# Optimization experiments

Hardware: AMD Instinct MI355X
Metric: run time of the kernel (lower is better)

The kernel has to match this reference:

```python
import jax, jax.numpy as jnp
import numpy as np

N, M, D, E = 16384, 8192, 8, 2_000_000
DELTA = 1.0   # init arg delta
P = 1.0       # init arg p (forced to 1 in __init__)
EPS = 1e-6


def setup_inputs() -> dict:
    key = jax.random.key(0)
    ks = jax.random.split(key, 7)
    return {
        "gamma_rows": jax.random.normal(ks[0], (N,), dtype=jnp.float32),
        "gamma_cols": jax.random.normal(ks[1], (M,), dtype=jnp.float32),
        "latent_z": jax.random.uniform(ks[2], (N, D), dtype=jnp.float32),
        "latent_w": jax.random.uniform(ks[3], (M, D), dtype=jnp.float32),
        "weights": jax.random.uniform(ks[4], (E,), dtype=jnp.float32),
        "rows_idx": jax.random.randint(ks[5], (E,), 0, N, dtype=jnp.int32),
        "col_idx": jax.random.randint(ks[6], (E,), 0, M, dtype=jnp.int32),
    }


def reference(gamma_rows, gamma_cols, latent_z, latent_w, weights, rows_idx, col_idx):
    # Simplex projections (Softmax over latent dim)
    z = jax.nn.softmax(latent_z, axis=1)   # [N, D]
    w = jax.nn.softmax(latent_w, axis=1)   # [M, D]

    # torch.cdist(z, w, p=2): full N x M euclidean distance matrix
    sq = (jnp.sum(z * z, axis=1)[:, None]
          + jnp.sum(w * w, axis=1)[None, :]
          - 2.0 * (z @ w.T))                       # [N, M]
    dist = jnp.sqrt(jnp.maximum(sq, 0.0))          # [N, M]
    dist_matrix = -DELTA * (dist + EPS)            # [N, M]

    # z_pdist1 = exp(gamma_rows) @ exp(dist_matrix) @ exp(gamma_cols)
    z_pdist1 = jnp.einsum("i,ij,j->", jnp.exp(gamma_rows),
                          jnp.exp(dist_matrix), jnp.exp(gamma_cols))

    # Edge (link) term: per-edge euclidean distance between gathered embeddings
    delta_latent = jnp.sqrt(jnp.sum((z[rows_idx] - w[col_idx]) ** 2, axis=-1))  # [E]
    z_pdist2 = jnp.sum(weights * (gamma_rows[rows_idx] + gamma_cols[col_idx]
                                  - (DELTA * delta_latent) ** P))

    return -z_pdist2 + z_pdist1
```

## Files before the change

kernel.cpp:

```cpp
#include <hip/hip_runtime.h>
#include <math.h>

#define N_ROWS 16384
#define M_COLS 8192
#define TPB 256
#define IT 4
#define JT 128
#define NJ (M_COLS / JT)
#define NIB (N_ROWS / (TPB * IT))
#define PAIR_BLOCKS (NIB * NJ)
#define EDGE_BLOCKS 1024
#define FUSED_BLOCKS (PAIR_BLOCKS + EDGE_BLOCKS)

typedef float v2f __attribute__((ext_vector_type(2)));

#define LOG2E 1.4426950408889634f
#define C2 2.0813689810056077f

__global__ __launch_bounds__(TPB) void rownorm_kernel(
    const float* __restrict__ lz, const float* __restrict__ gr,
    const float* __restrict__ lw, const float* __restrict__ gc,
    float* __restrict__ z, float* __restrict__ zz, float* __restrict__ eg,
    float* __restrict__ w, float* __restrict__ ww, float* __restrict__ ec)
{
    int gi = blockIdx.x * TPB + threadIdx.x;
    const float *src, *g;
    float *dv, *dq, *de;
    int i;
    if (gi < N_ROWS) { src = lz; g = gr; dv = z; dq = zz; de = eg; i = gi; }
    else             { src = lw; g = gc; dv = w; dq = ww; de = ec; i = gi - N_ROWS; }

    const float4* sp = (const float4*)(src + (size_t)i * 8);
    float4 a = sp[0], b = sp[1];
    float v[8] = {a.x, a.y, a.z, a.w, b.x, b.y, b.z, b.w};
    float m = v[0];
    #pragma unroll
    for (int d = 1; d < 8; d++) m = fmaxf(m, v[d]);
    float s = 0.f;
    #pragma unroll
    for (int d = 0; d < 8; d++) { v[d] = __expf(v[d] - m); s += v[d]; }
    float inv = 1.f / s;
    float sq = 0.f;
    #pragma unroll
    for (int d = 0; d < 8; d++) { v[d] *= inv; sq = fmaf(v[d], v[d], sq); }
    float4 o0 = {v[0], v[1], v[2], v[3]};
    float4 o1 = {v[4], v[5], v[6], v[7]};
    float4* dp = (float4*)(dv + (size_t)i * 8);
    dp[0] = o0; dp[1] = o1;
    dq[i] = C2 * sq;
    de[i] = __expf(g[i]);
}

__global__ __launch_bounds__(TPB) void fused_kernel(
    const float* __restrict__ z, const float* __restrict__ zz,
    const float* __restrict__ eg,
    const float* __restrict__ w, const float* __restrict__ ww,
    const float* __restrict__ ec,
    const float* __restrict__ gr, const float* __restrict__ gc,
    const float* __restrict__ wt,
    const int* __restrict__ ridx, const int* __restrict__ cidx, int E,
    double* __restrict__ pair_part, double* __restrict__ edge_part)
{
    __shared__ float  sw[JT * 8];
    __shared__ float  swq[JT];
    __shared__ float  sec[JT];
    __shared__ double sred[TPB];

    const int t   = threadIdx.x;
    const int rid = blockIdx.x >> 1;

    if ((blockIdx.x & 1) == 0) {
        const int ib = rid / NJ;
        const int jb = rid - ib * NJ;
        const int j0 = jb * JT;

        ((float4*)sw)[t] = ((const float4*)(w + (size_t)j0 * 8))[t];
        if (t < JT) { swq[t] = ww[j0 + t]; sec[t] = ec[j0 + t]; }

        v2f  zi[IT][4];
        float zzi[IT], acc[IT];
        const int ibase = ib * (TPB * IT);
        #pragma unroll
        for (int k = 0; k < IT; k++) {
            int i = ibase + k * TPB + t;
            const float4* zp = (const float4*)(z + (size_t)i * 8);
            float4 a = zp[0], b = zp[1];
            zi[k][0] = (v2f){-2.f * C2 * a.x, -2.f * C2 * a.y};
            zi[k][1] = (v2f){-2.f * C2 * a.z, -2.f * C2 * a.w};
            zi[k][2] = (v2f){-2.f * C2 * b.x, -2.f * C2 * b.y};
            zi[k][3] = (v2f){-2.f * C2 * b.z, -2.f * C2 * b.w};
            zzi[k] = zz[i];
            acc[k] = 0.f;
        }
        __syncthreads();

        for (int j = 0; j < JT; j++) {
            float4 wa = ((const float4*)sw)[j * 2];
            float4 wb = ((const float4*)sw)[j * 2 + 1];
            v2f w01 = {wa.x, wa.y}, w23 = {wa.z, wa.w};
            v2f w45 = {wb.x, wb.y}, w67 = {wb.z, wb.w};
            float wq = swq[j];
            float e  = sec[j];
            #pragma unroll
            for (int k = 0; k < IT; k++) {
                v2f p = {zzi[k], wq};
                p = __builtin_elementwise_fma(zi[k][0], w01, p);
                p = __builtin_elementwise_fma(zi[k][1], w23, p);
                p = __builtin_elementwise_fma(zi[k][2], w45, p);
                p = __builtin_elementwise_fma(zi[k][3], w67, p);
                float sq = fmaxf(p.x + p.y, 0.f);
                float d, pr;
                asm("v_sqrt_f32 %0, %1" : "=v"(d) : "v"(sq));
                asm("v_exp_f32 %0, -%1" : "=v"(pr) : "v"(d));
                acc[k] = fmaf(e, pr, acc[k]);
            }
        }

        double tp = 0.0;
        #pragma unroll
        for (int k = 0; k < IT; k++) {
            int i = ibase + k * TPB + t;
            tp += (double)eg[i] * (double)acc[k];
        }

        sred[t] = tp;
        __syncthreads();
        for (int s = TPB / 2; s > 0; s >>= 1) {
            if (t < s) sred[t] += sred[t + s];
            __syncthreads();
        }
        if (t == 0) pair_part[rid] = sred[0];
    } else {
        int tid = rid * TPB + t;
        const int stride = EDGE_BLOCKS * TPB;
        double local = 0.0;
        #pragma unroll 2
        for (int e = tid; e < E; e += stride) {
            int r = ridx[e], c = cidx[e];
            const float4* zp = (const float4*)(z + (size_t)r * 8);
            const float4* wp = (const float4*)(w + (size_t)c * 8);
            float4 za = zp[0], zb = zp[1], wa = wp[0], wb = wp[1];
            float d0 = za.x - wa.x, d1 = za.y - wa.y, d2 = za.z - wa.z, d3 = za.w - wa.w;
            float d4 = zb.x - wb.x, d5 = zb.y - wb.y, d6 = zb.z - wb.z, d7 = zb.w - wb.w;
            float s = d0 * d0;
            s = fmaf(d1, d1, s); s = fmaf(d2, d2, s); s = fmaf(d3, d3, s);
            s = fmaf(d4, d4, s); s = fmaf(d5, d5, s); s = fmaf(d6, d6, s);
            s = fmaf(d7, d7, s);
            float dist;
            asm("v_sqrt_f32 %0, %1" : "=v"(dist) : "v"(s));
            local += (double)(wt[e] * (gr[r] + gc[c] - dist));
        }
        sred[t] = local;
        __syncthreads();
        for (int s2 = TPB / 2; s2 > 0; s2 >>= 1) {
            if (t < s2) sred[t] += sred[t + s2];
            __syncthreads();
        }
        if (t == 0) edge_part[rid] = sred[0];
    }
}

__global__ __launch_bounds__(TPB) void final_kernel(
    const double* __restrict__ pp, int np,
    const double* __restrict__ ep, int ne,
    float* __restrict__ out)
{
    __shared__ double sred[TPB];
    const int t = threadIdx.x;
    double s1 = 0.0, s2 = 0.0;
    for (int i = t; i < np; i += TPB) s1 += pp[i];
    for (int i = t; i < ne; i += TPB) s2 += ep[i];
    sred[t] = s1;
    __syncthreads();
    for (int s = TPB / 2; s > 0; s >>= 1) {
        if (t < s) sred[t] += sred[t + s];
        __syncthreads();
    }
    double pair_sum = sred[0];
    __syncthreads();
    sred[t] = s2;
    __syncthreads();
    for (int s = TPB / 2; s > 0; s >>= 1) {
        if (t < s) sred[t] += sred[t + s];
        __syncthreads();
    }
    if (t == 0) {
        double edge_sum = sred[0];
        double cf = exp(-1.0e-6);
        out[0] = (float)(cf * pair_sum - edge_sum);
    }
}

extern "C" void kernel_launch(void* const* d_in, const int* in_sizes, int n_in,
                              void* d_out, int out_size, void* d_ws, size_t ws_size,
                              hipStream_t stream)
{
    const float* gamma_rows = (const float*)d_in[0];
    const float* gamma_cols = (const float*)d_in[1];
    const float* latent_z   = (const float*)d_in[2];
    const float* latent_w   = (const float*)d_in[3];
    const float* weights    = (const float*)d_in[4];
    const int*   rows_idx   = (const int*)d_in[5];
    const int*   col_idx    = (const int*)d_in[6];
    float* out = (float*)d_out;
    const int E = in_sizes[4];

    char* base = (char*)d_ws;
    size_t off = 0;
    float* z  = (float*)(base + off); off += (size_t)N_ROWS * 8 * 4;
    float* zz = (float*)(base + off); off += (size_t)N_ROWS * 4;
    float* eg = (float*)(base + off); off += (size_t)N_ROWS * 4;
    float* w  = (float*)(base + off); off += (size_t)M_COLS * 8 * 4;
    float* ww = (float*)(base + off); off += (size_t)M_COLS * 4;
    float* ec = (float*)(base + off); off += (size_t)M_COLS * 4;
    double* pair_part = (double*)(base + off); off += (size_t)PAIR_BLOCKS * 8;
    double* edge_part = (double*)(base + off); off += (size_t)EDGE_BLOCKS * 8;
    (void)ws_size;

    rownorm_kernel<<<(N_ROWS + M_COLS) / TPB, TPB, 0, stream>>>(
        latent_z, gamma_rows, latent_w, gamma_cols, z, zz, eg, w, ww, ec);
    fused_kernel<<<FUSED_BLOCKS, TPB, 0, stream>>>(
        z, zz, eg, w, ww, ec, gamma_rows, gamma_cols,
        weights, rows_idx, col_idx, E, pair_part, edge_part);
    final_kernel<<<1, TPB, 0, stream>>>(pair_part, PAIR_BLOCKS,
                                        edge_part, EDGE_BLOCKS, out);
}
```

Measured before the change: 173.4 us.

## Gather half-precision embeddings for edges, unroll edge loop, prefetch pair LDS reads

The row-normalisation kernel now also writes FP16 copies of the softmaxed embeddings. The edge path gathers those, with four edges per thread through vector loads of the index, weight and gamma values, so each random gather fetches half the bytes and more loads are in flight at once. Blocks are now interleaved one pair block to two edge blocks, and edge blocks double to 2048 so a single pass covers all edges. The pair loop prefetches the next column's shared-memory values and splits the FMA chain to shorten the dependency. The cost is FP16 rounding error in per-edge distances, and the single-pass edge path assumes E fits the grid and is a multiple of four.

Result: no change. 173.6 us (+0.1%).

```diff
diff --git a/kernel.cpp b/kernel.cpp
--- a/kernel.cpp
+++ b/kernel.cpp
@@ -9,26 +9,30 @@
 #define NJ (M_COLS / JT)
 #define NIB (N_ROWS / (TPB * IT))
 #define PAIR_BLOCKS (NIB * NJ)
-#define EDGE_BLOCKS 1024
-#define FUSED_BLOCKS (PAIR_BLOCKS + EDGE_BLOCKS)
+#define EDGE_BLOCKS 2048
+#define EU 4
+#define GRID_BLOCKS (PAIR_BLOCKS + EDGE_BLOCKS)
 
 typedef float v2f __attribute__((ext_vector_type(2)));
-
-#define LOG2E 1.4426950408889634f
+typedef _Float16 h8 __attribute__((ext_vector_type(8)));
+
 #define C2 2.0813689810056077f
 
 __global__ __launch_bounds__(TPB) void rownorm_kernel(
     const float* __restrict__ lz, const float* __restrict__ gr,
     const float* __restrict__ lw, const float* __restrict__ gc,
     float* __restrict__ z, float* __restrict__ zz, float* __restrict__ eg,
-    float* __restrict__ w, float* __restrict__ ww, float* __restrict__ ec)
+    _Float16* __restrict__ zh,
+    float* __restrict__ w, float* __restrict__ ww, float* __restrict__ ec,
+    _Float16* __restrict__ wh)
 {
     int gi = blockIdx.x * TPB + threadIdx.x;
     const float *src, *g;
     float *dv, *dq, *de;
+    _Float16* dh;
     int i;
-    if (gi < N_ROWS) { src = lz; g = gr; dv = z; dq = zz; de = eg; i = gi; }
-    else             { src = lw; g = gc; dv = w; dq = ww; de = ec; i = gi - N_ROWS; }
+    if (gi < N_ROWS) { src = lz; g = gr; dv = z; dq = zz; de = eg; dh = zh; i = gi; }
+    else             { src = lw; g = gc; dv = w; dq = ww; de = ec; dh = wh; i = gi - N_ROWS; }
 
     const float4* sp = (const float4*)(src + (size_t)i * 8);
     float4 a = sp[0], b = sp[1];
@@ -41,12 +45,18 @@
     for (int d = 0; d < 8; d++) { v[d] = __expf(v[d] - m); s += v[d]; }
     float inv = 1.f / s;
     float sq = 0.f;
+    h8 hv;
     #pragma unroll
-    for (int d = 0; d < 8; d++) { v[d] *= inv; sq = fmaf(v[d], v[d], sq); }
+    for (int d = 0; d < 8; d++) {
+        v[d] *= inv;
+        sq = fmaf(v[d], v[d], sq);
+        hv[d] = (_Float16)v[d];
+    }
     float4 o0 = {v[0], v[1], v[2], v[3]};
     float4 o1 = {v[4], v[5], v[6], v[7]};
     float4* dp = (float4*)(dv + (size_t)i * 8);
     dp[0] = o0; dp[1] = o1;
+    *(h8*)(dh + (size_t)i * 8) = hv;
     dq[i] = C2 * sq;
     de[i] = __expf(g[i]);
 }
@@ -56,6 +66,7 @@
     const float* __restrict__ eg,
     const float* __restrict__ w, const float* __restrict__ ww,
     const float* __restrict__ ec,
+    const _Float16* __restrict__ zh, const _Float16* __restrict__ wh,
     const float* __restrict__ gr, const float* __restrict__ gc,
     const float* __restrict__ wt,
     const int* __restrict__ ridx, const int* __restrict__ cidx, int E,
@@ -66,10 +77,13 @@
     __shared__ float  sec[JT];
     __shared__ double sred[TPB];
 
-    const int t   = threadIdx.x;
-    const int rid = blockIdx.x >> 1;
-
-    if ((blockIdx.x & 1) == 0) {
+    const int t     = threadIdx.x;
+    const int bid   = blockIdx.x;
+    const int third = bid / 3;
+    const int rem   = bid - third * 3;
+
+    if (rem == 0) {
+        const int rid = third;
         const int ib = rid / NJ;
         const int jb = rid - ib * NJ;
         const int j0 = jb * JT;
@@ -94,26 +108,31 @@
         }
         __syncthreads();
 
+        const float4* s4 = (const float4*)sw;
+        float4 wa = s4[0], wb = s4[1];
+        float wq = swq[0], e = sec[0];
         for (int j = 0; j < JT; j++) {
-            float4 wa = ((const float4*)sw)[j * 2];
-            float4 wb = ((const float4*)sw)[j * 2 + 1];
+            const int jn = (j + 1) & (JT - 1);
+            float4 wan = s4[jn * 2], wbn = s4[jn * 2 + 1];
+            float wqn = swq[jn], en = sec[jn];
+
             v2f w01 = {wa.x, wa.y}, w23 = {wa.z, wa.w};
             v2f w45 = {wb.x, wb.y}, w67 = {wb.z, wb.w};
-            float wq = swq[j];
-            float e  = sec[j];
             #pragma unroll
             for (int k = 0; k < IT; k++) {
                 v2f p = {zzi[k], wq};
                 p = __builtin_elementwise_fma(zi[k][0], w01, p);
                 p = __builtin_elementwise_fma(zi[k][1], w23, p);
-                p = __builtin_elementwise_fma(zi[k][2], w45, p);
-                p = __builtin_elementwise_fma(zi[k][3], w67, p);
+                v2f q = zi[k][2] * w45;
+                q = __builtin_elementwise_fma(zi[k][3], w67, q);
+                p += q;
                 float sq = fmaxf(p.x + p.y, 0.f);
                 float d, pr;
                 asm("v_sqrt_f32 %0, %1" : "=v"(d) : "v"(sq));
                 asm("v_exp_f32 %0, -%1" : "=v"(pr) : "v"(d));
                 acc[k] = fmaf(e, pr, acc[k]);
             }
+            wa = wan; wb = wbn; wq = wqn; e = en;
         }
 
         double tp = 0.0;
@@ -131,24 +150,39 @@
         }
         if (t == 0) pair_part[rid] = sred[0];
     } else {
-        int tid = rid * TPB + t;
-        const int stride = EDGE_BLOCKS * TPB;
+        const int erank = 2 * third + (rem - 1);
+        const int tid = erank * TPB + t;
+        const int e0 = tid * EU;
         double local = 0.0;
-        #pragma unroll 2
-        for (int e = tid; e < E; e += stride) {
-            int r = ridx[e], c = cidx[e];
-            const float4* zp = (const float4*)(z + (size_t)r * 8);
-            const float4* wp = (const float4*)(w + (size_t)c * 8);
-            float4 za = zp[0], zb = zp[1], wa = wp[0], wb = wp[1];
-            float d0 = za.x - wa.x, d1 = za.y - wa.y, d2 = za.z - wa.z, d3 = za.w - wa.w;
-            float d4 = zb.x - wb.x, d5 = zb.y - wb.y, d6 = zb.z - wb.z, d7 = zb.w - wb.w;
-            float s = d0 * d0;
-            s = fmaf(d1, d1, s); s = fmaf(d2, d2, s); s = fmaf(d3, d3, s);
-            s = fmaf(d4, d4, s); s = fmaf(d5, d5, s); s = fmaf(d6, d6, s);
-            s = fmaf(d7, d7, s);
-            float dist;
-            asm("v_sqrt_f32 %0, %1" : "=v"(dist) : "v"(s));
-            local += (double)(wt[e] * (gr[r] + gc[c] - dist));
+        if (e0 < E) {
+            int4   rr  = *(const int4*)(ridx + e0);
+            int4   cc  = *(const int4*)(cidx + e0);
+            float4 wt4 = *(const float4*)(wt + e0);
+            int   r[EU]  = {rr.x, rr.y, rr.z, rr.w};
+            int   c[EU]  = {cc.x, cc.y, cc.z, cc.w};
+            float wv[EU] = {wt4.x, wt4.y, wt4.z, wt4.w};
+            h8 zr[EU], wr[EU];
+            float grv[EU], gcv[EU];
+            #pragma unroll
+            for (int u = 0; u < EU; u++) {
+                zr[u]  = *(const h8*)(zh + (size_t)r[u] * 8);
+                wr[u]  = *(const h8*)(wh + (size_t)c[u] * 8);
+                grv[u] = gr[r[u]];
+                gcv[u] = gc[c[u]];
+            }
+            #pragma unroll
+            for (int u = 0; u < EU; u++) {
+                h8 dv = zr[u] - wr[u];
+                float s = 0.f;
+                #pragma unroll
+                for (int qd = 0; qd < 8; qd++) {
+                    float f = (float)dv[qd];
+                    s = fmaf(f, f, s);
+                }
+                float dist;
+                asm("v_sqrt_f32 %0, %1" : "=v"(dist) : "v"(s));
+                local += (double)(wv[u] * (grv[u] + gcv[u] - dist));
+            }
         }
         sred[t] = local;
         __syncthreads();
@@ -156,7 +190,7 @@
             if (t < s2) sred[t] += sred[t + s2];
             __syncthreads();
         }
-        if (t == 0) edge_part[rid] = sred[0];
+        if (t == 0) edge_part[erank] = sred[0];
     }
 }
 
@@ -213,14 +247,17 @@
     float* w  = (float*)(base + off); off += (size_t)M_COLS * 8 * 4;
     float* ww = (float*)(base + off); off += (size_t)M_COLS * 4;
     float* ec = (float*)(base + off); off += (size_t)M_COLS * 4;
+    _Float16* zh = (_Float16*)(base + off); off += (size_t)N_ROWS * 8 * 2;
+    _Float16* wh = (_Float16*)(base + off); off += (size_t)M_COLS * 8 * 2;
     double* pair_part = (double*)(base + off); off += (size_t)PAIR_BLOCKS * 8;
     double* edge_part = (double*)(base + off); off += (size_t)EDGE_BLOCKS * 8;
     (void)ws_size;
 
     rownorm_kernel<<<(N_ROWS + M_COLS) / TPB, TPB, 0, stream>>>(
-        latent_z, gamma_rows, latent_w, gamma_cols, z, zz, eg, w, ww, ec);
-    fused_kernel<<<FUSED_BLOCKS, TPB, 0, stream>>>(
-        z, zz, eg, w, ww, ec, gamma_rows, gamma_cols,
+        latent_z, gamma_rows, latent_w, gamma_cols,
+        z, zz, eg, zh, w, ww, ec, wh);
+    fused_kernel<<<GRID_BLOCKS, TPB, 0, stream>>>(
+        z, zz, eg, w, ww, ec, zh, wh, gamma_rows, gamma_cols,
         weights, rows_idx, col_idx, E, pair_part, edge_part);
     final_kernel<<<1, TPB, 0, stream>>>(pair_part, PAIR_BLOCKS,
                                         edge_part, EDGE_BLOCKS, out);
```
